# Performance work log

Hardware: AMD Instinct MI355X
Metric: run time of the kernel (lower is better)

The kernel has to match this reference:

```python
import jax, jax.numpy as jnp
import numpy as np

EPS = 1e-5

def setup_inputs() -> dict:
    key = jax.random.key(0)
    ks = jax.random.split(key, 5)
    B, C, H, W = 8, 128, 56, 56
    mid, out_c = 64, 256
    x1 = jax.random.normal(ks[0], (B, C, H, W), dtype=jnp.float32)
    x2 = jax.random.normal(ks[1], (B, C, H, W), dtype=jnp.float32)
    # 1x1 conv weights stored as (out, in); scaled like kaiming-ish init
    W1 = jax.random.normal(ks[2], (mid, C), dtype=jnp.float32) * (1.0 / np.sqrt(C))
    W2 = jax.random.normal(ks[3], (mid, C), dtype=jnp.float32) * (1.0 / np.sqrt(C))
    # interaction_proj weight (out_c, mid*mid) reshaped to (out_c, mid, mid);
    # index order matches torch reshape(B, c*mid + d, H, W)
    Wp = jax.random.normal(ks[4], (out_c, mid, mid), dtype=jnp.float32) * (1.0 / mid)
    gamma = jnp.ones((out_c,), dtype=jnp.float32)
    beta = jnp.zeros((out_c,), dtype=jnp.float32)
    return {"x1": x1, "x2": x2, "W1": W1, "W2": W2, "Wp": Wp, "gamma": gamma, "beta": beta}


def reference(x1, x2, W1, W2, Wp, gamma, beta):
    # 1x1 conv projections: (B,C,H,W) x (mid,C) -> (B,mid,H,W)
    p1 = jnp.einsum('bchw,mc->bmhw', x1, W1)
    p2 = jnp.einsum('bchw,dc->bdhw', x2, W2)
    # per-pixel outer product covar[b,c,d,h,w] = p1[b,c]*p2[b,d], then
    # 1x1 conv contraction over the mid^2 channel: fused as one einsum
    out = jnp.einsum('bchw,bdhw,ocd->bohw', p1, p2, Wp)
    # LayerNorm over channel dim (applied in NHWC in the original)
    x = jnp.transpose(out, (0, 2, 3, 1))  # B,H,W,out_c
    mu = jnp.mean(x, axis=-1, keepdims=True)
    var = jnp.mean(jnp.square(x - mu), axis=-1, keepdims=True)
    x = (x - mu) / jnp.sqrt(var + EPS) * gamma + beta
    x = jnp.transpose(x, (0, 3, 1, 2))  # back to B,out_c,H,W
    # torch nn.GELU() default is exact (erf) gelu
    return jax.nn.gelu(x, approximate=False)
```

## Files before the change

### kernel.cpp

```cpp
#include <hip/hip_runtime.h>

typedef unsigned short u16;
typedef __bf16 bf16x8 __attribute__((ext_vector_type(8)));
typedef float f32x4 __attribute__((ext_vector_type(4)));
typedef unsigned short u16x8 __attribute__((ext_vector_type(8)));
typedef unsigned short u16x4 __attribute__((ext_vector_type(4)));

#define NPIX 25088
#define HW 3136

static __device__ __forceinline__ u16 f2bf(float f) {
  unsigned u = __builtin_bit_cast(unsigned, f);
  return (u16)((u + 0x7fffu + ((u >> 16) & 1u)) >> 16);
}
static __device__ __forceinline__ float bf2f(u16 h) {
  return __builtin_bit_cast(float, ((unsigned)h) << 16);
}

__global__ __launch_bounds__(256) void prep_kernel(
    const float* __restrict__ Wp, const float* __restrict__ W1,
    const float* __restrict__ W2,
    u16* __restrict__ Wpb, u16* __restrict__ W1b, u16* __restrict__ W2b)
{
  const int blk = blockIdx.x;
  const int t = threadIdx.x;

  if (blk < 512) {
    const long e = (long)blk * 2048 + (long)t * 8;
    f32x4 a = *(const f32x4*)(Wp + e);
    f32x4 b = *(const f32x4*)(Wp + e + 4);
    u16x8 v;
    v[0]=f2bf(a[0]); v[1]=f2bf(a[1]); v[2]=f2bf(a[2]); v[3]=f2bf(a[3]);
    v[4]=f2bf(b[0]); v[5]=f2bf(b[1]); v[6]=f2bf(b[2]); v[7]=f2bf(b[3]);
    const int o = (int)(e >> 12);
    const int c = (int)(e >> 6) & 63;
    const int j = (int)(e >> 3) & 7;
    *(u16x8*)(Wpb + c * 16384 + o * 64 + ((j ^ (o & 7)) << 3)) = v;
  } else {
    const int e = (blk - 512) * 2048 + t * 8;
    const bool is1 = e < 8192;
    const float* src = is1 ? (W1 + e) : (W2 + e - 8192);
    u16* dst = is1 ? (W1b + e) : (W2b + e - 8192);
    f32x4 a = *(const f32x4*)(src);
    f32x4 b = *(const f32x4*)(src + 4);
    u16x8 v;
    v[0]=f2bf(a[0]); v[1]=f2bf(a[1]); v[2]=f2bf(a[2]); v[3]=f2bf(a[3]);
    v[4]=f2bf(b[0]); v[5]=f2bf(b[1]); v[6]=f2bf(b[2]); v[7]=f2bf(b[3]);
    *(u16x8*)dst = v;
  }
}

__global__ __launch_bounds__(128) void proj_kernel(
    const float* __restrict__ x1, const float* __restrict__ x2,
    const u16* __restrict__ W1b, const u16* __restrict__ W2b,
    u16* __restrict__ P1b, u16* __restrict__ P2b)
{
  const int t = threadIdx.x;
  const int br = t >> 6;
  const int lane = t & 63;
  const int l15 = lane & 15;
  const int l4 = lane >> 4;
  const int P0 = blockIdx.x * 64;

  const float* __restrict__ x = br ? x2 : x1;
  const u16* __restrict__ Wb = br ? W2b : W1b;

  size_t xbase[4];
  #pragma unroll
  for (int m = 0; m < 4; ++m) {
    const int px = P0 + m * 16 + l15;
    const int b = px / HW;
    const int hw = px - b * HW;
    xbase[m] = (size_t)b * 128 * HW + hw;
  }

  const f32x4 zero4 = {0.f, 0.f, 0.f, 0.f};
  f32x4 acc[4][4];
  #pragma unroll
  for (int m = 0; m < 4; ++m)
    #pragma unroll
    for (int n = 0; n < 4; ++n) acc[m][n] = zero4;

  #pragma unroll 1
  for (int ks = 0; ks < 4; ++ks) {
    const int k0 = ks * 32 + l4 * 8;
    bf16x8 afr[4];
    #pragma unroll
    for (int m = 0; m < 4; ++m) {
      u16x8 av;
      #pragma unroll
      for (int j = 0; j < 8; ++j)
        av[j] = f2bf(x[xbase[m] + (size_t)(k0 + j) * HW]);
      afr[m] = __builtin_bit_cast(bf16x8, av);
    }
    bf16x8 bfr[4];
    #pragma unroll
    for (int n = 0; n < 4; ++n)
      bfr[n] = __builtin_bit_cast(bf16x8,
          *(const u16x8*)(Wb + (n * 16 + l15) * 128 + k0));
    #pragma unroll
    for (int m = 0; m < 4; ++m)
      #pragma unroll
      for (int n = 0; n < 4; ++n)
        acc[m][n] = __builtin_amdgcn_mfma_f32_16x16x32_bf16(afr[m], bfr[n],
                                                            acc[m][n], 0, 0, 0);
  }

  if (br == 0) {
    #pragma unroll
    for (int m = 0; m < 4; ++m)
      #pragma unroll
      for (int n = 0; n < 4; ++n) {
        u16x4 v;
        #pragma unroll
        for (int r = 0; r < 4; ++r) v[r] = f2bf(acc[m][n][r]);
        *(u16x4*)(P1b + (size_t)(n * 16 + l15) * NPIX + P0 + m * 16 + l4 * 4) = v;
      }
  } else {
    #pragma unroll
    for (int m = 0; m < 4; ++m)
      #pragma unroll
      for (int n = 0; n < 4; ++n)
        #pragma unroll
        for (int r = 0; r < 4; ++r)
          P2b[(size_t)(P0 + m * 16 + l4 * 4 + r) * 64 + n * 16 + l15] =
              f2bf(acc[m][n][r]);
  }
}

__global__ __launch_bounds__(512, 2) void mm_kernel(
    const u16* __restrict__ P1b, const u16* __restrict__ P2b,
    const u16* __restrict__ Wpb, const float* __restrict__ gamma,
    const float* __restrict__ beta, float* __restrict__ out)
{
  __shared__ __align__(16) unsigned char smem[91136];
  u16*   P1s   = (u16*)smem;
  u16*   Bbuf0 = (u16*)(smem + 16384);
  u16*   Bbuf1 = (u16*)(smem + 49152);
  float* ssum  = (float*)(smem + 81920);
  float* ssq   = (float*)(smem + 86016);
  float* smean = (float*)(smem + 90112);
  float* srstd = (float*)(smem + 90624);

  const int t = threadIdx.x;
  const int w = t >> 6;
  const int lane = t & 63;
  const int l15 = lane & 15;
  const int l4 = lane >> 4;
  const int P0 = blockIdx.x * 128;

  {
    const int c = t >> 3, col = (t & 7) * 16;
    *(u16x8*)&P1s[c * 128 + col] =
        *(const u16x8*)(P1b + (size_t)c * NPIX + P0 + col);
    *(u16x8*)&P1s[c * 128 + col + 8] =
        *(const u16x8*)(P1b + (size_t)c * NPIX + P0 + col + 8);
  }

  bf16x8 afr[8][2];
  #pragma unroll
  for (int m = 0; m < 8; ++m)
    #pragma unroll
    for (int ks = 0; ks < 2; ++ks)
      afr[m][ks] = __builtin_bit_cast(bf16x8,
          *(const u16x8*)(P2b + (size_t)(P0 + m * 16 + l15) * 64
                          + ks * 32 + l4 * 8));

#define STAGE(DST, CS) {                                                        \
    const u16* src_ = Wpb + (size_t)(CS) * 16384;                               \
    _Pragma("unroll")                                                           \
    for (int i_ = 0; i_ < 4; ++i_) {                                            \
      const int off_ = (w * 4 + i_) * 512;                                      \
      __builtin_amdgcn_global_load_lds(                                         \
          (const __attribute__((address_space(1))) unsigned*)(src_ + off_ + lane * 8), \
          (__attribute__((address_space(3))) unsigned*)((DST) + off_),          \
          16, 0, 0);                                                            \
    }                                                                           \
  }

  STAGE(Bbuf0, 0);

  unsigned bofs[2][2];
  #pragma unroll
  for (int n = 0; n < 2; ++n) {
    const int o = w * 32 + n * 16 + l15;
    #pragma unroll
    for (int ks = 0; ks < 2; ++ks)
      bofs[n][ks] = (unsigned)(o * 64 + (((ks * 4 + l4) ^ (o & 7)) << 3));
  }

  const f32x4 zero4 = {0.f, 0.f, 0.f, 0.f};
  f32x4 acc[8][2];
  #pragma unroll
  for (int m = 0; m < 8; ++m)
    #pragma unroll
    for (int n = 0; n < 2; ++n) acc[m][n] = zero4;

  __syncthreads();

  #pragma unroll 2
  for (int c = 0; c < 64; ++c) {
    u16* Bc = (c & 1) ? Bbuf1 : Bbuf0;
    if (c < 63) STAGE(((c & 1) ? Bbuf0 : Bbuf1), c + 1);

    bf16x8 bfr[2][2];
    #pragma unroll
    for (int n = 0; n < 2; ++n)
      #pragma unroll
      for (int ks = 0; ks < 2; ++ks)
        bfr[n][ks] = __builtin_bit_cast(bf16x8, *(const u16x8*)&Bc[bofs[n][ks]]);

    float p1f[8][4];
    #pragma unroll
    for (int m = 0; m < 8; ++m) {
      u16x4 pv = *(const u16x4*)&P1s[c * 128 + m * 16 + l4 * 4];
      #pragma unroll
      for (int r = 0; r < 4; ++r) p1f[m][r] = bf2f(pv[r]);
    }

    #pragma unroll
    for (int m = 0; m < 8; ++m)
      #pragma unroll
      for (int n = 0; n < 2; ++n) {
        f32x4 s = zero4;
        s = __builtin_amdgcn_mfma_f32_16x16x32_bf16(afr[m][0], bfr[n][0], s, 0, 0, 0);
        s = __builtin_amdgcn_mfma_f32_16x16x32_bf16(afr[m][1], bfr[n][1], s, 0, 0, 0);
        #pragma unroll
        for (int r = 0; r < 4; ++r)
          acc[m][n][r] = fmaf(p1f[m][r], s[r], acc[m][n][r]);
      }

    __syncthreads();
  }

  float psum[8][4], psq[8][4];
  #pragma unroll
  for (int m = 0; m < 8; ++m)
    #pragma unroll
    for (int r = 0; r < 4; ++r) {
      float a0 = acc[m][0][r], a1 = acc[m][1][r];
      psum[m][r] = a0 + a1;
      psq[m][r]  = a0 * a0 + a1 * a1;
    }
  #pragma unroll
  for (int mask = 1; mask < 16; mask <<= 1) {
    #pragma unroll
    for (int m = 0; m < 8; ++m)
      #pragma unroll
      for (int r = 0; r < 4; ++r) {
        psum[m][r] += __shfl_xor(psum[m][r], mask);
        psq[m][r]  += __shfl_xor(psq[m][r], mask);
      }
  }
  if (l15 == 0) {
    #pragma unroll
    for (int m = 0; m < 8; ++m)
      #pragma unroll
      for (int r = 0; r < 4; ++r) {
        const int px = m * 16 + l4 * 4 + r;
        ssum[px * 8 + w] = psum[m][r];
        ssq[px * 8 + w]  = psq[m][r];
      }
  }
  __syncthreads();

  if (t < 128) {
    f32x4 s0 = *(const f32x4*)&ssum[t * 8];
    f32x4 s1 = *(const f32x4*)&ssum[t * 8 + 4];
    f32x4 q0 = *(const f32x4*)&ssq[t * 8];
    f32x4 q1 = *(const f32x4*)&ssq[t * 8 + 4];
    float s = s0[0]+s0[1]+s0[2]+s0[3] + s1[0]+s1[1]+s1[2]+s1[3];
    float q = q0[0]+q0[1]+q0[2]+q0[3] + q1[0]+q1[1]+q1[2]+q1[3];
    float mu = s * (1.f / 256.f);
    float var = q * (1.f / 256.f) - mu * mu;
    smean[t] = mu;
    srstd[t] = rsqrtf(var + 1e-5f);
  }
  __syncthreads();

  f32x4 mean[8], rstd[8];
  #pragma unroll
  for (int m = 0; m < 8; ++m) {
    mean[m] = *(const f32x4*)&smean[m * 16 + l4 * 4];
    rstd[m] = *(const f32x4*)&srstd[m * 16 + l4 * 4];
  }

  int bimg[2], hwl[2];
  #pragma unroll
  for (int h = 0; h < 2; ++h) {
    const int pxg = P0 + h * 64 + lane;
    bimg[h] = pxg / HW;
    hwl[h] = pxg - bimg[h] * HW;
  }

  float* tbuf = (float*)(smem + w * 8512);

  #pragma unroll
  for (int n = 0; n < 2; ++n) {
    const int obase = w * 32 + n * 16;
    const float gam = gamma[obase + l15];
    const float bet = beta[obase + l15];
    __syncthreads();
    #pragma unroll
    for (int m = 0; m < 8; ++m)
      #pragma unroll
      for (int r = 0; r < 4; ++r) {
        float v = (acc[m][n][r] - mean[m][r]) * rstd[m][r];
        v = v * gam + bet;
        const float ge = 0.5f * v * (1.f + erff(v * 0.70710678f));
        tbuf[l15 * 133 + m * 16 + l4 * 4 + r] = ge;
      }
    __syncthreads();
    #pragma unroll
    for (int row = 0; row < 16; ++row) {
      const int o = obase + row;
      #pragma unroll
      for (int h = 0; h < 2; ++h) {
        const float v = tbuf[row * 133 + h * 64 + lane];
        out[(size_t)bimg[h] * 802816 + (size_t)o * HW + hwl[h]] = v;
      }
    }
  }
#undef STAGE
}

extern "C" void kernel_launch(void* const* d_in, const int* in_sizes, int n_in,
                              void* d_out, int out_size, void* d_ws, size_t ws_size,
                              hipStream_t stream) {
  const float* x1    = (const float*)d_in[0];
  const float* x2    = (const float*)d_in[1];
  const float* W1    = (const float*)d_in[2];
  const float* W2    = (const float*)d_in[3];
  const float* Wp    = (const float*)d_in[4];
  const float* gamma = (const float*)d_in[5];
  const float* beta  = (const float*)d_in[6];
  float* out = (float*)d_out;

  u16* P1b = (u16*)d_ws;
  u16* P2b = (u16*)((char*)d_ws + 3211264);
  u16* Wpb = (u16*)((char*)d_ws + 6422528);
  u16* W1b = (u16*)((char*)d_ws + 8519680);
  u16* W2b = (u16*)((char*)d_ws + 8536064);

  prep_kernel<<<dim3(520), dim3(256), 0, stream>>>(Wp, W1, W2, Wpb, W1b, W2b);
  proj_kernel<<<dim3(392), dim3(128), 0, stream>>>(x1, x2, W1b, W2b, P1b, P2b);
  mm_kernel<<<dim3(196), dim3(512), 0, stream>>>(P1b, P2b, Wpb, gamma, beta, out);
}
```

Baseline: 175.5 us.

## Fuse weight prep into projection kernel and halve mm tile for occupancy

Merges the weight-conversion and projection kernels into one launch, with the projection converting W1/W2 from fp32 on the fly instead of reading pre-converted bf16 copies. The main matmul kernel now handles 64 pixels per block instead of 128 and launches 392 blocks. This is meant to remove one launch and fill the GPU's CUs better than the old 196-block grid. The cost is that each block streams the full Wp tensor for only half as many pixels, which doubles Wp traffic.

```diff
diff --git a/kernel.cpp b/kernel.cpp
--- a/kernel.cpp
+++ b/kernel.cpp
@@ -17,16 +17,17 @@
   return __builtin_bit_cast(float, ((unsigned)h) << 16);
 }
 
-__global__ __launch_bounds__(256) void prep_kernel(
-    const float* __restrict__ Wp, const float* __restrict__ W1,
-    const float* __restrict__ W2,
-    u16* __restrict__ Wpb, u16* __restrict__ W1b, u16* __restrict__ W2b)
+__global__ __launch_bounds__(256, 2) void prep_proj_kernel(
+    const float* __restrict__ x1, const float* __restrict__ x2,
+    const float* __restrict__ W1, const float* __restrict__ W2,
+    const float* __restrict__ Wp,
+    u16* __restrict__ P1b, u16* __restrict__ P2b, u16* __restrict__ Wpb)
 {
   const int blk = blockIdx.x;
   const int t = threadIdx.x;
 
-  if (blk < 512) {
-    const long e = (long)blk * 2048 + (long)t * 8;
+  if (blk >= 196) {
+    const long e = (long)(blk - 196) * 2048 + (long)t * 8;
     f32x4 a = *(const f32x4*)(Wp + e);
     f32x4 b = *(const f32x4*)(Wp + e + 4);
     u16x8 v;
@@ -36,34 +37,19 @@
     const int c = (int)(e >> 6) & 63;
     const int j = (int)(e >> 3) & 7;
     *(u16x8*)(Wpb + c * 16384 + o * 64 + ((j ^ (o & 7)) << 3)) = v;
-  } else {
-    const int e = (blk - 512) * 2048 + t * 8;
-    const bool is1 = e < 8192;
-    const float* src = is1 ? (W1 + e) : (W2 + e - 8192);
-    u16* dst = is1 ? (W1b + e) : (W2b + e - 8192);
-    f32x4 a = *(const f32x4*)(src);
-    f32x4 b = *(const f32x4*)(src + 4);
-    u16x8 v;
-    v[0]=f2bf(a[0]); v[1]=f2bf(a[1]); v[2]=f2bf(a[2]); v[3]=f2bf(a[3]);
-    v[4]=f2bf(b[0]); v[5]=f2bf(b[1]); v[6]=f2bf(b[2]); v[7]=f2bf(b[3]);
-    *(u16x8*)dst = v;
-  }
-}
-
-__global__ __launch_bounds__(128) void proj_kernel(
-    const float* __restrict__ x1, const float* __restrict__ x2,
-    const u16* __restrict__ W1b, const u16* __restrict__ W2b,
-    u16* __restrict__ P1b, u16* __restrict__ P2b)
-{
-  const int t = threadIdx.x;
-  const int br = t >> 6;
+    return;
+  }
+
+  const int w = t >> 6;
+  const int br = w & 1;
+  const int h = w >> 1;
   const int lane = t & 63;
   const int l15 = lane & 15;
   const int l4 = lane >> 4;
-  const int P0 = blockIdx.x * 64;
+  const int P0 = blk * 128 + h * 64;
 
   const float* __restrict__ x = br ? x2 : x1;
-  const u16* __restrict__ Wb = br ? W2b : W1b;
+  const float* __restrict__ Wf = br ? W2 : W1;
 
   size_t xbase[4];
   #pragma unroll
@@ -95,9 +81,14 @@
     }
     bf16x8 bfr[4];
     #pragma unroll
-    for (int n = 0; n < 4; ++n)
-      bfr[n] = __builtin_bit_cast(bf16x8,
-          *(const u16x8*)(Wb + (n * 16 + l15) * 128 + k0));
+    for (int n = 0; n < 4; ++n) {
+      f32x4 w0 = *(const f32x4*)(Wf + (n * 16 + l15) * 128 + k0);
+      f32x4 w1 = *(const f32x4*)(Wf + (n * 16 + l15) * 128 + k0 + 4);
+      u16x8 bv;
+      bv[0]=f2bf(w0[0]); bv[1]=f2bf(w0[1]); bv[2]=f2bf(w0[2]); bv[3]=f2bf(w0[3]);
+      bv[4]=f2bf(w1[0]); bv[5]=f2bf(w1[1]); bv[6]=f2bf(w1[2]); bv[7]=f2bf(w1[3]);
+      bfr[n] = __builtin_bit_cast(bf16x8, bv);
+    }
     #pragma unroll
     for (int m = 0; m < 4; ++m)
       #pragma unroll
@@ -128,38 +119,33 @@
   }
 }
 
-__global__ __launch_bounds__(512, 2) void mm_kernel(
+__global__ __launch_bounds__(512, 4) void mm_kernel(
     const u16* __restrict__ P1b, const u16* __restrict__ P2b,
     const u16* __restrict__ Wpb, const float* __restrict__ gamma,
     const float* __restrict__ beta, float* __restrict__ out)
 {
-  __shared__ __align__(16) unsigned char smem[91136];
+  __shared__ __align__(16) unsigned char smem[78336];
   u16*   P1s   = (u16*)smem;
-  u16*   Bbuf0 = (u16*)(smem + 16384);
-  u16*   Bbuf1 = (u16*)(smem + 49152);
-  float* ssum  = (float*)(smem + 81920);
-  float* ssq   = (float*)(smem + 86016);
-  float* smean = (float*)(smem + 90112);
-  float* srstd = (float*)(smem + 90624);
+  u16*   Bbuf0 = (u16*)(smem + 8192);
+  u16*   Bbuf1 = (u16*)(smem + 40960);
+  float* ssum  = (float*)(smem + 73728);
+  float* ssq   = (float*)(smem + 75776);
+  float* smean = (float*)(smem + 77824);
+  float* srstd = (float*)(smem + 78080);
 
   const int t = threadIdx.x;
   const int w = t >> 6;
   const int lane = t & 63;
   const int l15 = lane & 15;
   const int l4 = lane >> 4;
-  const int P0 = blockIdx.x * 128;
-
-  {
-    const int c = t >> 3, col = (t & 7) * 16;
-    *(u16x8*)&P1s[c * 128 + col] =
-        *(const u16x8*)(P1b + (size_t)c * NPIX + P0 + col);
-    *(u16x8*)&P1s[c * 128 + col + 8] =
-        *(const u16x8*)(P1b + (size_t)c * NPIX + P0 + col + 8);
-  }
-
-  bf16x8 afr[8][2];
-  #pragma unroll
-  for (int m = 0; m < 8; ++m)
+  const int P0 = blockIdx.x * 64;
+
+  *(u16x8*)&P1s[(t >> 3) * 64 + (t & 7) * 8] =
+      *(const u16x8*)(P1b + (size_t)(t >> 3) * NPIX + P0 + (t & 7) * 8);
+
+  bf16x8 afr[4][2];
+  #pragma unroll
+  for (int m = 0; m < 4; ++m)
     #pragma unroll
     for (int ks = 0; ks < 2; ++ks)
       afr[m][ks] = __builtin_bit_cast(bf16x8,
@@ -190,9 +176,9 @@
   }
 
   const f32x4 zero4 = {0.f, 0.f, 0.f, 0.f};
-  f32x4 acc[8][2];
-  #pragma unroll
-  for (int m = 0; m < 8; ++m)
+  f32x4 acc[4][2];
+  #pragma unroll
+  for (int m = 0; m < 4; ++m)
     #pragma unroll
     for (int n = 0; n < 2; ++n) acc[m][n] = zero4;
 
@@ -210,16 +196,16 @@
       for (int ks = 0; ks < 2; ++ks)
         bfr[n][ks] = __builtin_bit_cast(bf16x8, *(const u16x8*)&Bc[bofs[n][ks]]);
 
-    float p1f[8][4];
-    #pragma unroll
-    for (int m = 0; m < 8; ++m) {
-      u16x4 pv = *(const u16x4*)&P1s[c * 128 + m * 16 + l4 * 4];
+    float p1f[4][4];
+    #pragma unroll
+    for (int m = 0; m < 4; ++m) {
+      u16x4 pv = *(const u16x4*)&P1s[c * 64 + m * 16 + l4 * 4];
       #pragma unroll
       for (int r = 0; r < 4; ++r) p1f[m][r] = bf2f(pv[r]);
     }
 
     #pragma unroll
-    for (int m = 0; m < 8; ++m)
+    for (int m = 0; m < 4; ++m)
       #pragma unroll
       for (int n = 0; n < 2; ++n) {
         f32x4 s = zero4;
@@ -233,9 +219,9 @@
     __syncthreads();
   }
 
-  float psum[8][4], psq[8][4];
-  #pragma unroll
-  for (int m = 0; m < 8; ++m)
+  float psum[4][4], psq[4][4];
+  #pragma unroll
+  for (int m = 0; m < 4; ++m)
     #pragma unroll
     for (int r = 0; r < 4; ++r) {
       float a0 = acc[m][0][r], a1 = acc[m][1][r];
@@ -245,7 +231,7 @@
   #pragma unroll
   for (int mask = 1; mask < 16; mask <<= 1) {
     #pragma unroll
-    for (int m = 0; m < 8; ++m)
+    for (int m = 0; m < 4; ++m)
       #pragma unroll
       for (int r = 0; r < 4; ++r) {
         psum[m][r] += __shfl_xor(psum[m][r], mask);
@@ -254,7 +240,7 @@
   }
   if (l15 == 0) {
     #pragma unroll
-    for (int m = 0; m < 8; ++m)
+    for (int m = 0; m < 4; ++m)
       #pragma unroll
       for (int r = 0; r < 4; ++r) {
         const int px = m * 16 + l4 * 4 + r;
@@ -264,7 +250,7 @@
   }
   __syncthreads();
 
-  if (t < 128) {
+  if (t < 64) {
     f32x4 s0 = *(const f32x4*)&ssum[t * 8];
     f32x4 s1 = *(const f32x4*)&ssum[t * 8 + 4];
     f32x4 q0 = *(const f32x4*)&ssq[t * 8];
@@ -278,22 +264,18 @@
   }
   __syncthreads();
 
-  f32x4 mean[8], rstd[8];
-  #pragma unroll
-  for (int m = 0; m < 8; ++m) {
+  f32x4 mean[4], rstd[4];
+  #pragma unroll
+  for (int m = 0; m < 4; ++m) {
     mean[m] = *(const f32x4*)&smean[m * 16 + l4 * 4];
     rstd[m] = *(const f32x4*)&srstd[m * 16 + l4 * 4];
   }
 
-  int bimg[2], hwl[2];
-  #pragma unroll
-  for (int h = 0; h < 2; ++h) {
-    const int pxg = P0 + h * 64 + lane;
-    bimg[h] = pxg / HW;
-    hwl[h] = pxg - bimg[h] * HW;
-  }
-
-  float* tbuf = (float*)(smem + w * 8512);
+  const int pxg = P0 + lane;
+  const int bimg = pxg / HW;
+  const int hwl = pxg - bimg * HW;
+
+  float* tbuf = (float*)(smem + w * 4160);
 
   #pragma unroll
   for (int n = 0; n < 2; ++n) {
@@ -302,23 +284,19 @@
     const float bet = beta[obase + l15];
     __syncthreads();
     #pragma unroll
-    for (int m = 0; m < 8; ++m)
+    for (int m = 0; m < 4; ++m)
       #pragma unroll
       for (int r = 0; r < 4; ++r) {
         float v = (acc[m][n][r] - mean[m][r]) * rstd[m][r];
         v = v * gam + bet;
         const float ge = 0.5f * v * (1.f + erff(v * 0.70710678f));
-        tbuf[l15 * 133 + m * 16 + l4 * 4 + r] = ge;
+        tbuf[l15 * 65 + m * 16 + l4 * 4 + r] = ge;
       }
     __syncthreads();
     #pragma unroll
     for (int row = 0; row < 16; ++row) {
       const int o = obase + row;
-      #pragma unroll
-      for (int h = 0; h < 2; ++h) {
-        const float v = tbuf[row * 133 + h * 64 + lane];
-        out[(size_t)bimg[h] * 802816 + (size_t)o * HW + hwl[h]] = v;
-      }
+      out[(size_t)bimg * 802816 + (size_t)o * HW + hwl] = tbuf[row * 65 + lane];
     }
   }
 #undef STAGE
@@ -339,10 +317,8 @@
   u16* P1b = (u16*)d_ws;
   u16* P2b = (u16*)((char*)d_ws + 3211264);
   u16* Wpb = (u16*)((char*)d_ws + 6422528);
-  u16* W1b = (u16*)((char*)d_ws + 8519680);
-  u16* W2b = (u16*)((char*)d_ws + 8536064);
-
-  prep_kernel<<<dim3(520), dim3(256), 0, stream>>>(Wp, W1, W2, Wpb, W1b, W2b);
-  proj_kernel<<<dim3(392), dim3(128), 0, stream>>>(x1, x2, W1b, W2b, P1b, P2b);
-  mm_kernel<<<dim3(196), dim3(512), 0, stream>>>(P1b, P2b, Wpb, gamma, beta, out);
-}
+
+  prep_proj_kernel<<<dim3(708), dim3(256), 0, stream>>>(x1, x2, W1, W2, Wp,
+                                                        P1b, P2b, Wpb);
+  mm_kernel<<<dim3(392), dim3(512), 0, stream>>>(P1b, P2b, Wpb, gamma, beta, out);
+}
```

Result: faster. 170.0 us (-3.1%).
